# Optimization experiments

Measured on AMD Instinct MI355X. Metric: run time of the kernel, lower is better.

The kernel has to match this reference:

```python
import jax, jax.numpy as jnp
import numpy as np

D_MODEL = 256
N_HEADS = 8


def setup_inputs() -> dict:
    key = jax.random.key(0)
    ks = jax.random.split(key, 12)
    B, S, d, H = 4, 1024, D_MODEL, N_HEADS
    s = 0.02
    return {
        "Q": jax.random.normal(ks[0], (B, S, d), jnp.float32),
        "K": jax.random.normal(ks[1], (B, S, d), jnp.float32),
        "V": jax.random.normal(ks[2], (B, S, d), jnp.float32),
        "Wq": jax.random.normal(ks[3], (d, d * H), jnp.float32) * s,
        "bq": jnp.zeros((d * H,), jnp.float32),
        "Wk": jax.random.normal(ks[4], (d, d * H), jnp.float32) * s,
        "bk": jnp.zeros((d * H,), jnp.float32),
        "Wv": jax.random.normal(ks[5], (d, d * H), jnp.float32) * s,
        "bv": jnp.zeros((d * H,), jnp.float32),
        "Wo": jax.random.normal(ks[6], (H * d, d), jnp.float32) * s,
        "bo": jnp.zeros((d,), jnp.float32),
    }


def reference(Q, K, V, Wq, bq, Wk, bk, Wv, bv, Wo, bo):
    B, S, d = Q.shape
    H = N_HEADS
    # projections: [B,S,d] -> [B,S,H*d] -> [B,H,S,d] (head_dim == d_model here)
    q = (Q @ Wq + bq).reshape(B, S, H, d).transpose(0, 2, 1, 3)
    k = (K @ Wk + bk).reshape(B, S, H, d).transpose(0, 2, 1, 3)
    v = (V @ Wv + bv).reshape(B, S, H, d).transpose(0, 2, 1, 3)
    scores = jnp.einsum("bhqd,bhkd->bhqk", q, k) / jnp.sqrt(jnp.float32(d))
    attn = jax.nn.softmax(scores, axis=-1)
    out = jnp.einsum("bhqk,bhkd->bhqd", attn, v)  # [B,H,S,d]
    out = out.transpose(0, 2, 1, 3).reshape(B, S, H * d)
    return out @ Wo + bo
```

## Files before the change

### kernel.cpp

```cpp
#include <hip/hip_runtime.h>
#include <stdint.h>

#define NB 4
#define SEQ 1024
#define DM 256
#define NH 8

typedef __attribute__((ext_vector_type(8))) short bf8;
typedef __attribute__((ext_vector_type(4))) float f4;

__device__ __forceinline__ unsigned short f2bf(float f) {
  union { float f; uint32_t u; } c; c.f = f;
  uint32_t u = c.u;
  return (unsigned short)((u + 0x7FFFu + ((u >> 16) & 1u)) >> 16);
}

__device__ __forceinline__ void gl_lds16(const unsigned short* g, short* l) {
  __builtin_amdgcn_global_load_lds(
      (const __attribute__((address_space(1))) unsigned int*)g,
      (__attribute__((address_space(3))) unsigned int*)l, 16, 0, 0);
}

__global__ __launch_bounds__(256) void prep_kernel(
    const float* __restrict__ Wq, const float* __restrict__ Wk,
    const float* __restrict__ Wv, const float* __restrict__ Wo,
    const float* __restrict__ Q, const float* __restrict__ K,
    const float* __restrict__ V,
    unsigned short* __restrict__ Wt3, unsigned short* __restrict__ WoT,
    unsigned short* __restrict__ Xbf) {
  const int z = blockIdx.y;
  const int tid = threadIdx.x;
  if (z >= 4) {
    const float* src = (z == 4) ? Q : (z == 5) ? K : V;
    const size_t off = (size_t)blockIdx.x * 1024 + tid * 4;
    const float4 v = *(const float4*)(src + off);
    short4 s;
    s.x = (short)f2bf(v.x); s.y = (short)f2bf(v.y);
    s.z = (short)f2bf(v.z); s.w = (short)f2bf(v.w);
    *(short4*)(Xbf + (size_t)(z - 4) * 4096 * 256 + off) = s;
    return;
  }
  if (blockIdx.x >= 512) return;
  const float* in;
  unsigned short* out;
  int R, C, bx, by;
  if (z < 3) {
    in = (z == 0) ? Wq : (z == 1) ? Wk : Wv;
    out = Wt3 + (size_t)z * 2048 * 256;
    R = 256; C = 2048; bx = blockIdx.x & 63; by = blockIdx.x >> 6;
  } else {
    in = Wo; out = WoT;
    R = 2048; C = 256; bx = blockIdx.x & 7; by = blockIdx.x >> 3;
  }
  __shared__ float t[32][33];
  const int c0 = bx * 32, r0 = by * 32;
  const int tx = tid & 31, ty = tid >> 5;
#pragma unroll
  for (int i = 0; i < 4; i++) {
    int r = r0 + ty + i * 8;
    t[ty + i * 8][tx] = in[(size_t)r * C + c0 + tx];
  }
  __syncthreads();
#pragma unroll
  for (int i = 0; i < 4; i++) {
    int c = c0 + ty + i * 8;
    out[(size_t)c * R + r0 + tx] = f2bf(t[tx][ty + i * 8]);
  }
}

__global__ __launch_bounds__(256) void proj_kernel(
    const unsigned short* __restrict__ Xbf, const unsigned short* __restrict__ Wt3,
    const float* __restrict__ bq, const float* __restrict__ bk, const float* __restrict__ bv,
    unsigned short* __restrict__ q_ws, unsigned short* __restrict__ k_ws,
    unsigned short* __restrict__ vT_ws) {
  const int z = blockIdx.z;
  const unsigned short* X = Xbf + (size_t)z * 4096 * 256;
  const unsigned short* Wt = Wt3 + (size_t)z * 2048 * 256;
  const float* bias = (z == 0) ? bq : (z == 1) ? bk : bv;

  __shared__ short a_lds[128 * 32];
  __shared__ short b_lds[128 * 32];

  const int tid = threadIdx.x;
  const int wid = tid >> 6, lane = tid & 63;
  const int quad = lane >> 4, l16 = lane & 15;
  const int wm = wid >> 1, wn = wid & 1;
  const int m0 = blockIdx.x * 128, n0 = blockIdx.y * 128;

  f4 acc[4][4];
  const f4 z4 = {0.f, 0.f, 0.f, 0.f};
#pragma unroll
  for (int i = 0; i < 4; i++)
#pragma unroll
    for (int j = 0; j < 4; j++) acc[i][j] = z4;

  const int srow = lane >> 2;
  const int schunk = lane & 3;
  const int cxor = quad ^ (l16 & 3);

  for (int ko = 0; ko < 8; ko++) {
    const int k0 = ko * 32;
#pragma unroll
    for (int j = 0; j < 2; j++) {
      const int i = wid * 2 + j;
      const int row = i * 16 + srow;
      const int sc = (schunk ^ (row & 3)) * 8;
      gl_lds16(X + (size_t)(m0 + row) * DM + k0 + sc, a_lds + i * 512);
      gl_lds16(Wt + (size_t)(n0 + row) * DM + k0 + sc, b_lds + i * 512);
    }
    __syncthreads();
    bf8 af[4], bfv[4];
#pragma unroll
    for (int mi = 0; mi < 4; mi++)
      af[mi] = *(const bf8*)(a_lds + (wm * 64 + mi * 16 + l16) * 32 + cxor * 8);
#pragma unroll
    for (int ni = 0; ni < 4; ni++)
      bfv[ni] = *(const bf8*)(b_lds + (wn * 64 + ni * 16 + l16) * 32 + cxor * 8);
#pragma unroll
    for (int mi = 0; mi < 4; mi++)
#pragma unroll
      for (int ni = 0; ni < 4; ni++)
        acc[mi][ni] = __builtin_amdgcn_mfma_f32_16x16x32_bf16(af[mi], bfv[ni], acc[mi][ni], 0, 0, 0);
    __syncthreads();
  }

  if (z < 2) {
    const float scale = (z == 0) ? 0.0625f : 1.0f;
    unsigned short* qk_out = (z == 0) ? q_ws : k_ws;
#pragma unroll
    for (int ni = 0; ni < 4; ni++) {
      const int n = n0 + wn * 64 + ni * 16 + l16;
      const float bsv = bias[n];
      const int h = n >> 8, j = n & 255;
#pragma unroll
      for (int mi = 0; mi < 4; mi++) {
#pragma unroll
        for (int reg = 0; reg < 4; reg++) {
          const int m = m0 + wm * 64 + mi * 16 + quad * 4 + reg;
          const int b = m >> 10, sr = m & 1023;
          qk_out[(((size_t)b * NH + h) * SEQ + sr) * DM + j] =
              f2bf((acc[mi][ni][reg] + bsv) * scale);
        }
      }
    }
  } else {
#pragma unroll
    for (int ni = 0; ni < 4; ni++) {
      const int n = n0 + wn * 64 + ni * 16 + l16;
      const float bsv = bias[n];
      const int h = n >> 8, j = n & 255;
#pragma unroll
      for (int mi = 0; mi < 4; mi++) {
        const int m = m0 + wm * 64 + mi * 16 + quad * 4;
        const int b = m >> 10, sr = m & 1023;
        short4 s4;
        s4.x = (short)f2bf(acc[mi][ni][0] + bsv);
        s4.y = (short)f2bf(acc[mi][ni][1] + bsv);
        s4.z = (short)f2bf(acc[mi][ni][2] + bsv);
        s4.w = (short)f2bf(acc[mi][ni][3] + bsv);
        *(short4*)(vT_ws + (((size_t)b * NH + h) * DM + j) * SEQ + sr) = s4;
      }
    }
  }
}

__global__ __launch_bounds__(512, 4) void attn_kernel(
    const unsigned short* __restrict__ q_ws, const unsigned short* __restrict__ k_ws,
    const unsigned short* __restrict__ vT_ws, unsigned short* __restrict__ o_ws) {
  __shared__ short q_lds[64][260];
  __shared__ short p_lds[64][264];
  __shared__ float l_sh[8][64];

  const int tid = threadIdx.x;
  const int wid = tid >> 6, lane = tid & 63;
  const int quad = lane >> 4, l16 = lane & 15;
  const int blk = blockIdx.x;
  const int g = blk & 7;
  const int qt = (blk >> 3) & 15;
  const int bh = g + 8 * (blk >> 7);
  const size_t qkbase = (size_t)bh * SEQ * DM;
  const size_t vbase = (size_t)bh * DM * SEQ;

  {
    const int sr = tid >> 3, sch = tid & 7;
    const unsigned short* src = q_ws + qkbase + (size_t)(qt * 64 + sr) * DM + sch * 32;
#pragma unroll
    for (int i = 0; i < 4; i++)
      *(bf8*)(&q_lds[sr][sch * 32 + i * 8]) = *(const bf8*)(src + i * 8);
  }

  const f4 z4 = {0.f, 0.f, 0.f, 0.f};
  f4 Oacc[2][4];
#pragma unroll
  for (int i = 0; i < 2; i++)
#pragma unroll
    for (int j = 0; j < 4; j++) Oacc[i][j] = z4;
  float lpart[4][4];
#pragma unroll
  for (int i = 0; i < 4; i++)
#pragma unroll
    for (int j = 0; j < 4; j++) lpart[i][j] = 0.f;

  __syncthreads();

  for (int sup = 0; sup < 4; sup++) {
    const int kvw = sup * 256 + wid * 32;
    f4 Sacc[4][2];
#pragma unroll
    for (int i = 0; i < 4; i++)
#pragma unroll
      for (int j = 0; j < 2; j++) Sacc[i][j] = z4;
#pragma unroll
    for (int kc = 0; kc < 8; kc++) {
      bf8 aq[4];
#pragma unroll
      for (int mi = 0; mi < 4; mi++)
        aq[mi] = *(const bf8*)(&q_lds[mi * 16 + l16][kc * 32 + quad * 8]);
#pragma unroll
      for (int ni = 0; ni < 2; ni++) {
        const bf8 kb = *(const bf8*)(k_ws + qkbase +
            (size_t)(kvw + ni * 16 + l16) * DM + kc * 32 + quad * 8);
#pragma unroll
        for (int mi = 0; mi < 4; mi++)
          Sacc[mi][ni] = __builtin_amdgcn_mfma_f32_16x16x32_bf16(aq[mi], kb, Sacc[mi][ni], 0, 0, 0);
      }
    }
    __syncthreads();
#pragma unroll
    for (int mi = 0; mi < 4; mi++)
#pragma unroll
      for (int reg = 0; reg < 4; reg++) {
        float s = 0.f;
#pragma unroll
        for (int ni = 0; ni < 2; ni++) {
          const float p = exp2f(Sacc[mi][ni][reg] * 1.44269504f);
          s += p;
          p_lds[mi * 16 + quad * 4 + reg][wid * 32 + ni * 16 + l16] = (short)f2bf(p);
        }
        lpart[mi][reg] += s;
      }
    __syncthreads();
#pragma unroll
    for (int kc2 = 0; kc2 < 8; kc2++) {
      bf8 av_[2], pb[4];
#pragma unroll
      for (int mi = 0; mi < 2; mi++)
        av_[mi] = *(const bf8*)(vT_ws + vbase +
            (size_t)(wid * 32 + mi * 16 + l16) * SEQ + sup * 256 + kc2 * 32 + quad * 8);
#pragma unroll
      for (int nq = 0; nq < 4; nq++)
        pb[nq] = *(const bf8*)(&p_lds[nq * 16 + l16][kc2 * 32 + quad * 8]);
#pragma unroll
      for (int mi = 0; mi < 2; mi++)
#pragma unroll
        for (int nq = 0; nq < 4; nq++)
          Oacc[mi][nq] = __builtin_amdgcn_mfma_f32_16x16x32_bf16(av_[mi], pb[nq], Oacc[mi][nq], 0, 0, 0);
    }
  }

#pragma unroll
  for (int mi = 0; mi < 4; mi++)
#pragma unroll
    for (int reg = 0; reg < 4; reg++) {
      float v = lpart[mi][reg];
      v += __shfl_xor(v, 1, 64);
      v += __shfl_xor(v, 2, 64);
      v += __shfl_xor(v, 4, 64);
      v += __shfl_xor(v, 8, 64);
      lpart[mi][reg] = v;
    }
  if (l16 == 0) {
#pragma unroll
    for (int mi = 0; mi < 4; mi++)
#pragma unroll
      for (int reg = 0; reg < 4; reg++)
        l_sh[wid][mi * 16 + quad * 4 + reg] = lpart[mi][reg];
  }
  __syncthreads();

  const int b = bh >> 3, h = bh & 7;
#pragma unroll
  for (int nq = 0; nq < 4; nq++) {
    const int q = nq * 16 + l16;
    float lsum = 0.f;
#pragma unroll
    for (int w = 0; w < 8; w++) lsum += l_sh[w][q];
    const float inv = 1.f / lsum;
    const size_t base = ((size_t)b * SEQ + qt * 64 + q) * (NH * DM) + h * DM + wid * 32;
#pragma unroll
    for (int mi = 0; mi < 2; mi++) {
      short4 s4;
      s4.x = (short)f2bf(Oacc[mi][nq][0] * inv);
      s4.y = (short)f2bf(Oacc[mi][nq][1] * inv);
      s4.z = (short)f2bf(Oacc[mi][nq][2] * inv);
      s4.w = (short)f2bf(Oacc[mi][nq][3] * inv);
      *(short4*)(o_ws + base + mi * 16 + quad * 4) = s4;
    }
  }
}

__global__ __launch_bounds__(256) void outproj_kernel(
    const unsigned short* __restrict__ o_ws, const unsigned short* __restrict__ WoT,
    const float* __restrict__ bo, float* __restrict__ out) {
  __shared__ short a_lds[32][136];
  __shared__ short b_lds[64][136];

  const int tid = threadIdx.x;
  const int wid = tid >> 6, lane = tid & 63;
  const int quad = lane >> 4, l16 = lane & 15;
  const int wm = wid & 1, wn = wid >> 1;
  const int m0 = blockIdx.x * 32, n0 = blockIdx.y * 64;

  const f4 z4 = {0.f, 0.f, 0.f, 0.f};
  f4 acc[2];
#pragma unroll
  for (int i = 0; i < 2; i++) acc[i] = z4;

  const int ch = tid & 15, row = tid >> 4;
  for (int ko = 0; ko < 16; ko++) {
    const int k0 = ko * 128;
#pragma unroll
    for (int rb = 0; rb < 2; rb++) {
      int r = row + rb * 16;
      *(bf8*)(&a_lds[r][ch * 8]) = *(const bf8*)(o_ws + (size_t)(m0 + r) * 2048 + k0 + ch * 8);
    }
#pragma unroll
    for (int rb = 0; rb < 4; rb++) {
      int r = row + rb * 16;
      *(bf8*)(&b_lds[r][ch * 8]) = *(const bf8*)(WoT + (size_t)(n0 + r) * 2048 + k0 + ch * 8);
    }
    __syncthreads();
#pragma unroll
    for (int kc = 0; kc < 4; kc++) {
      const bf8 af = *(const bf8*)(&a_lds[wm * 16 + l16][kc * 32 + quad * 8]);
      bf8 bfv[2];
#pragma unroll
      for (int ni = 0; ni < 2; ni++)
        bfv[ni] = *(const bf8*)(&b_lds[wn * 32 + ni * 16 + l16][kc * 32 + quad * 8]);
#pragma unroll
      for (int ni = 0; ni < 2; ni++)
        acc[ni] = __builtin_amdgcn_mfma_f32_16x16x32_bf16(af, bfv[ni], acc[ni], 0, 0, 0);
    }
    __syncthreads();
  }
#pragma unroll
  for (int ni = 0; ni < 2; ni++) {
    const int n = n0 + wn * 32 + ni * 16 + l16;
    const float bv = bo[n];
#pragma unroll
    for (int reg = 0; reg < 4; reg++) {
      const int m = m0 + wm * 16 + quad * 4 + reg;
      out[(size_t)m * DM + n] = acc[ni][reg] + bv;
    }
  }
}

extern "C" void kernel_launch(void* const* d_in, const int* in_sizes, int n_in,
                              void* d_out, int out_size, void* d_ws, size_t ws_size,
                              hipStream_t stream) {
  const float* Q  = (const float*)d_in[0];
  const float* K  = (const float*)d_in[1];
  const float* V  = (const float*)d_in[2];
  const float* Wq = (const float*)d_in[3];
  const float* bq = (const float*)d_in[4];
  const float* Wk = (const float*)d_in[5];
  const float* bk = (const float*)d_in[6];
  const float* Wv = (const float*)d_in[7];
  const float* bv = (const float*)d_in[8];
  const float* Wo = (const float*)d_in[9];
  const float* bo = (const float*)d_in[10];
  float* out = (float*)d_out;

  char* ws = (char*)d_ws;
  const size_t QS = (size_t)NB * NH * SEQ * DM * 2;
  unsigned short* q_ws  = (unsigned short*)(ws);
  unsigned short* k_ws  = (unsigned short*)(ws + QS);
  unsigned short* vT_ws = (unsigned short*)(ws + 2 * QS);
  unsigned short* o_ws  = (unsigned short*)(ws + 3 * QS);
  const size_t WT = (size_t)2048 * 256 * 2;
  unsigned short* Wt3 = (unsigned short*)(ws + 4 * QS);
  unsigned short* WoT = (unsigned short*)(ws + 4 * QS + 3 * WT);
  unsigned short* Xbf = o_ws;

  prep_kernel<<<dim3(1024, 7), 256, 0, stream>>>(Wq, Wk, Wv, Wo, Q, K, V,
                                                 Wt3, WoT, Xbf);
  proj_kernel<<<dim3(32, 16, 3), 256, 0, stream>>>(Xbf, Wt3, bq, bk, bv,
                                                   q_ws, k_ws, vT_ws);
  attn_kernel<<<512, 512, 0, stream>>>(q_ws, k_ws, vT_ws, o_ws);
  outproj_kernel<<<dim3(128, 4), 256, 0, stream>>>(o_ws, WoT, bo, out);
}
```

Measured before the change: 206.8 us.

## Store Q/K/V in MFMA fragment order and widen attention waves to 64 keys

```diff
diff --git a/kernel.cpp b/kernel.cpp
--- a/kernel.cpp
+++ b/kernel.cpp
@@ -20,6 +20,7 @@
       (const __attribute__((address_space(1))) unsigned int*)g,
       (__attribute__((address_space(3))) unsigned int*)l, 16, 0, 0);
 }
+
 
 __global__ __launch_bounds__(256) void prep_kernel(
     const float* __restrict__ Wq, const float* __restrict__ Wk,
@@ -71,8 +72,8 @@
 __global__ __launch_bounds__(256) void proj_kernel(
     const unsigned short* __restrict__ Xbf, const unsigned short* __restrict__ Wt3,
     const float* __restrict__ bq, const float* __restrict__ bk, const float* __restrict__ bv,
-    unsigned short* __restrict__ q_ws, unsigned short* __restrict__ k_ws,
-    unsigned short* __restrict__ vT_ws) {
+    unsigned short* __restrict__ q_frag, unsigned short* __restrict__ k_frag,
+    unsigned short* __restrict__ v_frag) {
   const int z = blockIdx.z;
   const unsigned short* X = Xbf + (size_t)z * 4096 * 256;
   const unsigned short* Wt = Wt3 + (size_t)z * 2048 * 256;
@@ -126,20 +127,22 @@
 
   if (z < 2) {
     const float scale = (z == 0) ? 0.0625f : 1.0f;
-    unsigned short* qk_out = (z == 0) ? q_ws : k_ws;
+    unsigned short* dst = (z == 0) ? q_frag : k_frag;
 #pragma unroll
     for (int ni = 0; ni < 4; ni++) {
       const int n = n0 + wn * 64 + ni * 16 + l16;
       const float bsv = bias[n];
-      const int h = n >> 8, j = n & 255;
+      const int h = n >> 8, d = n & 255;
+      const int dpart = (d >> 5) * 512 + (16 * ((d >> 3) & 3)) * 8 + (d & 7);
 #pragma unroll
       for (int mi = 0; mi < 4; mi++) {
 #pragma unroll
         for (int reg = 0; reg < 4; reg++) {
           const int m = m0 + wm * 64 + mi * 16 + quad * 4 + reg;
           const int b = m >> 10, sr = m & 1023;
-          qk_out[(((size_t)b * NH + h) * SEQ + sr) * DM + j] =
-              f2bf((acc[mi][ni][reg] + bsv) * scale);
+          const size_t idx = ((size_t)(b * NH + h) * 64 + (sr >> 4)) * 4096 +
+                             dpart + (sr & 15) * 8;
+          dst[idx] = f2bf((acc[mi][ni][reg] + bsv) * scale);
         }
       }
     }
@@ -148,28 +151,30 @@
     for (int ni = 0; ni < 4; ni++) {
       const int n = n0 + wn * 64 + ni * 16 + l16;
       const float bsv = bias[n];
-      const int h = n >> 8, j = n & 255;
+      const int h = n >> 8, d = n & 255;
 #pragma unroll
       for (int mi = 0; mi < 4; mi++) {
         const int m = m0 + wm * 64 + mi * 16 + quad * 4;
         const int b = m >> 10, sr = m & 1023;
+        const size_t idx = ((size_t)(b * NH + h) * 16 + (d >> 4)) * 16384 +
+                           (size_t)(sr >> 5) * 512 +
+                           ((d & 15) + 16 * ((sr >> 3) & 3)) * 8 + (sr & 7);
         short4 s4;
         s4.x = (short)f2bf(acc[mi][ni][0] + bsv);
         s4.y = (short)f2bf(acc[mi][ni][1] + bsv);
         s4.z = (short)f2bf(acc[mi][ni][2] + bsv);
         s4.w = (short)f2bf(acc[mi][ni][3] + bsv);
-        *(short4*)(vT_ws + (((size_t)b * NH + h) * DM + j) * SEQ + sr) = s4;
+        *(short4*)(v_frag + idx) = s4;
       }
     }
   }
 }
 
-__global__ __launch_bounds__(512, 4) void attn_kernel(
-    const unsigned short* __restrict__ q_ws, const unsigned short* __restrict__ k_ws,
-    const unsigned short* __restrict__ vT_ws, unsigned short* __restrict__ o_ws) {
-  __shared__ short q_lds[64][260];
+__global__ __launch_bounds__(256, 2) void attn_kernel(
+    const unsigned short* __restrict__ q_frag, const unsigned short* __restrict__ k_frag,
+    const unsigned short* __restrict__ v_frag, unsigned short* __restrict__ o_ws) {
   __shared__ short p_lds[64][264];
-  __shared__ float l_sh[8][64];
+  __shared__ float l_sh[4][64];
 
   const int tid = threadIdx.x;
   const int wid = tid >> 6, lane = tid & 63;
@@ -178,21 +183,19 @@
   const int g = blk & 7;
   const int qt = (blk >> 3) & 15;
   const int bh = g + 8 * (blk >> 7);
-  const size_t qkbase = (size_t)bh * SEQ * DM;
-  const size_t vbase = (size_t)bh * DM * SEQ;
-
+  const size_t fbase = (size_t)bh * 262144;
+
+  bf8 qf[8];
   {
-    const int sr = tid >> 3, sch = tid & 7;
-    const unsigned short* src = q_ws + qkbase + (size_t)(qt * 64 + sr) * DM + sch * 32;
-#pragma unroll
-    for (int i = 0; i < 4; i++)
-      *(bf8*)(&q_lds[sr][sch * 32 + i * 8]) = *(const bf8*)(src + i * 8);
+    const unsigned short* qp = q_frag + fbase + (size_t)(qt * 4 + wid) * 4096 + lane * 8;
+#pragma unroll
+    for (int kc = 0; kc < 8; kc++) qf[kc] = *(const bf8*)(qp + kc * 512);
   }
 
   const f4 z4 = {0.f, 0.f, 0.f, 0.f};
-  f4 Oacc[2][4];
-#pragma unroll
-  for (int i = 0; i < 2; i++)
+  f4 Oacc[4][4];
+#pragma unroll
+  for (int i = 0; i < 4; i++)
 #pragma unroll
     for (int j = 0; j < 4; j++) Oacc[i][j] = z4;
   float lpart[4][4];
@@ -201,28 +204,43 @@
 #pragma unroll
     for (int j = 0; j < 4; j++) lpart[i][j] = 0.f;
 
-  __syncthreads();
-
   for (int sup = 0; sup < 4; sup++) {
-    const int kvw = sup * 256 + wid * 32;
-    f4 Sacc[4][2];
+    f4 Sacc[4][4];
 #pragma unroll
     for (int i = 0; i < 4; i++)
 #pragma unroll
-      for (int j = 0; j < 2; j++) Sacc[i][j] = z4;
+      for (int j = 0; j < 4; j++) Sacc[i][j] = z4;
+    const unsigned short* kp = k_frag + fbase +
+        (size_t)(sup * 16 + wid * 4) * 4096 + lane * 8;
 #pragma unroll
     for (int kc = 0; kc < 8; kc++) {
-      bf8 aq[4];
-#pragma unroll
-      for (int mi = 0; mi < 4; mi++)
-        aq[mi] = *(const bf8*)(&q_lds[mi * 16 + l16][kc * 32 + quad * 8]);
-#pragma unroll
-      for (int ni = 0; ni < 2; ni++) {
-        const bf8 kb = *(const bf8*)(k_ws + qkbase +
-            (size_t)(kvw + ni * 16 + l16) * DM + kc * 32 + quad * 8);
+#pragma unroll
+      for (int ni = 0; ni < 4; ni++) {
+        const bf8 kb = *(const bf8*)(kp + (size_t)ni * 4096 + kc * 512);
 #pragma unroll
         for (int mi = 0; mi < 4; mi++)
-          Sacc[mi][ni] = __builtin_amdgcn_mfma_f32_16x16x32_bf16(aq[mi], kb, Sacc[mi][ni], 0, 0, 0);
+          Sacc[mi][ni] = __builtin_amdgcn_mfma_f32_16x16x32_bf16(qf[kc], kb, Sacc[mi][ni], 0, 0, 0);
+      }
+    }
+#pragma unroll
+    for (int i = 0; i < 4; i++)
+#pragma unroll
+      for (int j = 0; j < 4; j++) Sacc[i][j] = z4;
+    {
+      const unsigned short* qpa = q_frag + fbase + (size_t)(qt * 4) * 4096 + lane * 8;
+#pragma unroll
+      for (int kc = 0; kc < 8; kc++) {
+        bf8 aq[4];
+#pragma unroll
+        for (int mi = 0; mi < 4; mi++)
+          aq[mi] = *(const bf8*)(qpa + (size_t)mi * 4096 + kc * 512);
+#pragma unroll
+        for (int ni = 0; ni < 4; ni++) {
+          const bf8 kb = *(const bf8*)(kp + (size_t)ni * 4096 + kc * 512);
+#pragma unroll
+          for (int mi = 0; mi < 4; mi++)
+            Sacc[mi][ni] = __builtin_amdgcn_mfma_f32_16x16x32_bf16(aq[mi], kb, Sacc[mi][ni], 0, 0, 0);
+        }
       }
     }
     __syncthreads();
@@ -232,26 +250,27 @@
       for (int reg = 0; reg < 4; reg++) {
         float s = 0.f;
 #pragma unroll
-        for (int ni = 0; ni < 2; ni++) {
+        for (int ni = 0; ni < 4; ni++) {
           const float p = exp2f(Sacc[mi][ni][reg] * 1.44269504f);
           s += p;
-          p_lds[mi * 16 + quad * 4 + reg][wid * 32 + ni * 16 + l16] = (short)f2bf(p);
+          p_lds[mi * 16 + quad * 4 + reg][wid * 64 + ni * 16 + l16] = (short)f2bf(p);
         }
         lpart[mi][reg] += s;
       }
     __syncthreads();
+    const unsigned short* vp = v_frag + fbase +
+        (size_t)(wid * 4) * 16384 + (size_t)(sup * 8) * 512 + lane * 8;
 #pragma unroll
     for (int kc2 = 0; kc2 < 8; kc2++) {
-      bf8 av_[2], pb[4];
-#pragma unroll
-      for (int mi = 0; mi < 2; mi++)
-        av_[mi] = *(const bf8*)(vT_ws + vbase +
-            (size_t)(wid * 32 + mi * 16 + l16) * SEQ + sup * 256 + kc2 * 32 + quad * 8);
+      bf8 av_[4], pb[4];
+#pragma unroll
+      for (int mi = 0; mi < 4; mi++)
+        av_[mi] = *(const bf8*)(vp + (size_t)mi * 16384 + kc2 * 512);
 #pragma unroll
       for (int nq = 0; nq < 4; nq++)
         pb[nq] = *(const bf8*)(&p_lds[nq * 16 + l16][kc2 * 32 + quad * 8]);
 #pragma unroll
-      for (int mi = 0; mi < 2; mi++)
+      for (int mi = 0; mi < 4; mi++)
 #pragma unroll
         for (int nq = 0; nq < 4; nq++)
           Oacc[mi][nq] = __builtin_amdgcn_mfma_f32_16x16x32_bf16(av_[mi], pb[nq], Oacc[mi][nq], 0, 0, 0);
@@ -282,13 +301,10 @@
 #pragma unroll
   for (int nq = 0; nq < 4; nq++) {
     const int q = nq * 16 + l16;
-    float lsum = 0.f;
-#pragma unroll
-    for (int w = 0; w < 8; w++) lsum += l_sh[w][q];
-    const float inv = 1.f / lsum;
-    const size_t base = ((size_t)b * SEQ + qt * 64 + q) * (NH * DM) + h * DM + wid * 32;
-#pragma unroll
-    for (int mi = 0; mi < 2; mi++) {
+    const float inv = 1.f / (l_sh[0][q] + l_sh[1][q] + l_sh[2][q] + l_sh[3][q]);
+    const size_t base = ((size_t)b * SEQ + qt * 64 + q) * (NH * DM) + h * DM + wid * 64;
+#pragma unroll
+    for (int mi = 0; mi < 4; mi++) {
       short4 s4;
       s4.x = (short)f2bf(Oacc[mi][nq][0] * inv);
       s4.y = (short)f2bf(Oacc[mi][nq][1] * inv);
@@ -373,10 +389,10 @@
 
   char* ws = (char*)d_ws;
   const size_t QS = (size_t)NB * NH * SEQ * DM * 2;
-  unsigned short* q_ws  = (unsigned short*)(ws);
-  unsigned short* k_ws  = (unsigned short*)(ws + QS);
-  unsigned short* vT_ws = (unsigned short*)(ws + 2 * QS);
-  unsigned short* o_ws  = (unsigned short*)(ws + 3 * QS);
+  unsigned short* q_frag = (unsigned short*)(ws);
+  unsigned short* k_frag = (unsigned short*)(ws + QS);
+  unsigned short* v_frag = (unsigned short*)(ws + 2 * QS);
+  unsigned short* o_ws   = (unsigned short*)(ws + 3 * QS);
   const size_t WT = (size_t)2048 * 256 * 2;
   unsigned short* Wt3 = (unsigned short*)(ws + 4 * QS);
   unsigned short* WoT = (unsigned short*)(ws + 4 * QS + 3 * WT);
@@ -385,7 +401,7 @@
   prep_kernel<<<dim3(1024, 7), 256, 0, stream>>>(Wq, Wk, Wv, Wo, Q, K, V,
                                                  Wt3, WoT, Xbf);
   proj_kernel<<<dim3(32, 16, 3), 256, 0, stream>>>(Xbf, Wt3, bq, bk, bv,
-                                                   q_ws, k_ws, vT_ws);
-  attn_kernel<<<512, 512, 0, stream>>>(q_ws, k_ws, vT_ws, o_ws);
+                                                   q_frag, k_frag, v_frag);
+  attn_kernel<<<512, 256, 0, stream>>>(q_frag, k_frag, v_frag, o_ws);
   outproj_kernel<<<dim3(128, 4), 256, 0, stream>>>(o_ws, WoT, bo, out);
 }
```

Result: no change. 207.6 us (+0.4%).
